# Optimization experiments

Measured on AMD Instinct MI355X. Metric: run time of the kernel, lower is better.

## Reference

```python
import jax, jax.numpy as jnp
import numpy as np

N = 50000
E = 800000
P = 16
H = 128
NUM_LAYERS = 2


def _lin_params(key, fan_in, fan_out):
    k1, k2 = jax.random.split(key)
    bound = 1.0 / np.sqrt(fan_in)
    W = jax.random.uniform(k1, (fan_in, fan_out), jnp.float32, -bound, bound)
    b = jax.random.uniform(k2, (fan_out,), jnp.float32, -bound, bound)
    return W, b


def setup_inputs() -> dict:
    key = jax.random.key(0)
    ks = jax.random.split(key, 16)
    h = jax.random.normal(ks[0], (N, P), jnp.float32)
    x = jax.random.normal(ks[1], (N, 2), jnp.float32)
    edge_index = jax.random.randint(ks[2], (2, E), 0, N, jnp.int32)
    emb_W, emb_b = _lin_params(ks[3], P, H)
    e_W1, e_b1 = _lin_params(ks[4], 2 * H + 1, H)
    e_W2, e_b2 = _lin_params(ks[5], H, H)
    n_W1, n_b1 = _lin_params(ks[6], 2 * H, H)
    n_W2, n_b2 = _lin_params(ks[7], H, H)
    v_W1, v_b1 = _lin_params(ks[8], H, H)
    v_W2, v_b2 = _lin_params(ks[9], H, 2)
    c_W1, c_b1 = _lin_params(ks[10], H, H)
    c_W2, c_b2 = _lin_params(ks[11], H, 1)
    return dict(h=h, x=x, edge_index=edge_index,
                emb_W=emb_W, emb_b=emb_b,
                e_W1=e_W1, e_b1=e_b1, e_W2=e_W2, e_b2=e_b2,
                n_W1=n_W1, n_b1=n_b1, n_W2=n_W2, n_b2=n_b2,
                v_W1=v_W1, v_b1=v_b1, v_W2=v_W2, v_b2=v_b2,
                c_W1=c_W1, c_b1=c_b1, c_W2=c_W2, c_b2=c_b2)


def _mlp(z, W1, b1, W2, b2):
    return jnp.maximum(z @ W1 + b1, 0.0) @ W2 + b2


def reference(h, x, edge_index, emb_W, emb_b,
              e_W1, e_b1, e_W2, e_b2,
              n_W1, n_b1, n_W2, n_b2,
              v_W1, v_b1, v_W2, v_b2,
              c_W1, c_b1, c_W2, c_b2):
    row, col = edge_index[0], edge_index[1]
    n_nodes = h.shape[0]
    # edge count per source node for scatter-mean (0-count nodes stay 0)
    cnt = jax.ops.segment_sum(jnp.ones((row.shape[0],), h.dtype), row,
                              num_segments=n_nodes)
    denom = jnp.maximum(cnt, 1.0)[:, None]

    h = h @ emb_W + emb_b  # [N, H]
    v = None
    for _ in range(NUM_LAYERS):
        rel_pos = x[row] - x[col]                         # [E, 2]
        rel_dist = jnp.sum(rel_pos ** 2, axis=-1, keepdims=True)  # [E, 1]
        rel_theta = jnp.arctan2(rel_pos[:, 1], rel_pos[:, 0])     # [E]
        rel_pos2 = rel_dist * jnp.stack(
            [jnp.cos(2.0 * rel_theta), jnp.sin(2.0 * rel_theta)], axis=1)  # [E, 2]
        edge_feat = jnp.concatenate([h[row], h[col], rel_dist], axis=-1)   # [E, 2H+1]
        m_ij = _mlp(edge_feat, e_W1, e_b1, e_W2, e_b2)    # [E, H] (dropout = eval identity)
        m_i = jax.ops.segment_sum(m_ij, row, num_segments=n_nodes)  # [N, H]
        h = h + _mlp(jnp.concatenate([h, m_i], axis=-1), n_W1, n_b1, n_W2, n_b2)
        v = _mlp(h, v_W1, v_b1, v_W2, v_b2)               # [N, 2]
        coord = _mlp(m_ij, c_W1, c_b1, c_W2, c_b2)        # [E, 1]
        scat = jax.ops.segment_sum(rel_pos2 * coord, row, num_segments=n_nodes)
        v = v + scat / denom                              # scatter-mean
    # F.normalize(p=2, dim=-1, eps=1e-12)
    norm = jnp.linalg.norm(v, axis=-1, keepdims=True)
    v = v / jnp.maximum(norm, 1e-12)
    return h, x, v
```

## Files before the change

### kernel.cpp

```cpp
#include <hip/hip_runtime.h>
#include <hip/hip_fp16.h>

typedef _Float16 f16;
typedef unsigned short u16;
typedef f16 f16x2 __attribute__((ext_vector_type(2)));
typedef f16 f16x8 __attribute__((ext_vector_type(8)));
typedef float f32x4 __attribute__((ext_vector_type(4)));

constexpr int N_NODES = 50000;
constexpr int E_EDGES = 800000;
constexpr int NBINS   = 50176;
constexpr int NBLK    = 196;

constexpr size_t OFF_DEG   = 0;
constexpr size_t OFF_LOCEX = 200704;
constexpr size_t OFF_BSUM  = 401408;
constexpr size_t OFF_BOFF  = 402432;
constexpr size_t OFF_FILL  = 403456;
constexpr size_t OFF_SCAT  = 604160;
constexpr size_t OFF_SROW  = 1004160;
constexpr size_t OFF_SCOL  = 2604160;
constexpr size_t OFF_ZSUM  = 4204160;
constexpr size_t ZSH_BYTES = (size_t)N_NODES * 128 * 2;
constexpr size_t ZS_BYTES  = (size_t)N_NODES * 128 * 4;
constexpr size_t OFF_APRE  = OFF_ZSUM + ZS_BYTES;
constexpr size_t OFF_BPRE  = OFF_APRE + (size_t)N_NODES * 128 * 2;
constexpr size_t OFF_CMB   = OFF_BPRE + (size_t)N_NODES * 128 * 2;
constexpr size_t OFF_WX    = OFF_CMB + 65536;
constexpr size_t OFF_BVEC  = OFF_WX + 65536;
constexpr size_t OFF_BX    = OFF_BVEC + 512;
constexpr size_t OFF_WSWZ  = OFF_BX + 512;

__device__ __forceinline__ void split_f(float x, f16& h, f16& l) {
    h = (f16)x;
    l = (f16)(x - (float)h);
}

__device__ __forceinline__ f32x4 mfma3(f16x8 ah, f16x8 al, f16x8 bh, f16x8 bl, f32x4 acc) {
    acc = __builtin_amdgcn_mfma_f32_16x16x32_f16(ah, bh, acc, 0, 0, 0);
    acc = __builtin_amdgcn_mfma_f32_16x16x32_f16(al, bh, acc, 0, 0, 0);
    acc = __builtin_amdgcn_mfma_f32_16x16x32_f16(ah, bl, acc, 0, 0, 0);
    return acc;
}

__device__ __forceinline__ void pk_atomic_add(f16* addr, float a0, float a1) {
    __half2 hv = __floats2half2_rn(a0, a1);
    unsafeAtomicAdd((__half2*)addr, hv);
}

__global__ __launch_bounds__(256) void compose_kernel(
    const float* __restrict__ eW2, const float* __restrict__ eb2,
    const float* __restrict__ nW1, const float* __restrict__ cW1,
    const float* __restrict__ cb1,
    float* __restrict__ Wcmb, float* __restrict__ Wx,
    float* __restrict__ bvec, float* __restrict__ bx)
{
    const int gid = blockIdx.x * 256 + threadIdx.x;
    if (gid < 16384) {
        const int k = gid >> 7, j = gid & 127;
        float s = 0.f;
        for (int t2 = 0; t2 < 128; ++t2) s += eW2[k * 128 + t2] * nW1[(128 + t2) * 128 + j];
        Wcmb[gid] = s;
    } else if (gid < 32768) {
        const int e = gid - 16384;
        const int k = e >> 7, j = e & 127;
        float s = 0.f;
        for (int t2 = 0; t2 < 128; ++t2) s += eW2[k * 128 + t2] * cW1[t2 * 128 + j];
        Wx[e] = s;
    } else if (gid < 32896) {
        const int j = gid - 32768;
        float s = 0.f;
        for (int k = 0; k < 128; ++k) s += eb2[k] * nW1[(128 + k) * 128 + j];
        bvec[j] = s;
    } else if (gid < 33024) {
        const int j = gid - 32896;
        float s = cb1[j];
        for (int k = 0; k < 128; ++k) s += eb2[k] * cW1[k * 128 + j];
        bx[j] = s;
    }
}

__global__ __launch_bounds__(256) void prep_kernel(
    const float* __restrict__ eW1, const float* __restrict__ nW1,
    const float* __restrict__ nW2, const float* __restrict__ vW1,
    const float* __restrict__ Wcmb, const float* __restrict__ Wx,
    f16* __restrict__ Wpres, f16* __restrict__ nW1cs,
    f16* __restrict__ nW2s, f16* __restrict__ vW1s, f16* __restrict__ Wxs)
{
    const int gid = blockIdx.x * 256 + threadIdx.x;
    int K32, e, which; f16* out;
    if (gid < 32768)       { which = 0; out = Wpres; K32 = 4; e = gid; }
    else if (gid < 65536)  { which = 1; out = nW1cs; K32 = 8; e = gid - 32768; }
    else if (gid < 81920)  { which = 2; out = nW2s;  K32 = 4; e = gid - 65536; }
    else if (gid < 98304)  { which = 3; out = vW1s;  K32 = 4; e = gid - 81920; }
    else                   { which = 4; out = Wxs;   K32 = 4; e = gid - 98304; }
    const int per = 512 * K32;
    const int ct = e / per, rem = e % per;
    const int kk = rem >> 9, lane = (rem >> 3) & 63, j = rem & 7;
    const int col = ct * 16 + (lane & 15);
    const int k = kk * 32 + ((lane >> 4) & 3) * 8 + j;
    float v;
    if (which == 0)      v = (col < 128) ? eW1[k * 128 + col] : eW1[(128 + k) * 128 + (col - 128)];
    else if (which == 1) v = (k < 128) ? nW1[k * 128 + col] : Wcmb[(k - 128) * 128 + col];
    else if (which == 2) v = nW2[k * 128 + col];
    else if (which == 3) v = vW1[k * 128 + col];
    else                 v = Wx[k * 128 + col];
    f16 h, l; split_f(v, h, l);
    const int base = ((ct * K32 + kk) * 2) * 512 + lane * 8 + j;
    out[base] = h;
    out[base + 512] = l;
}

__global__ __launch_bounds__(256) void hist_kernel(const int* __restrict__ eidx,
                                                   int* __restrict__ deg) {
    const int e = blockIdx.x * 256 + threadIdx.x;
    if (e < E_EDGES) atomicAdd(&deg[eidx[e]], 1);
}

__global__ __launch_bounds__(256) void scan1_kernel(const int* __restrict__ deg,
                                                    int* __restrict__ locEx,
                                                    int* __restrict__ blockSum) {
    __shared__ int s[256];
    const int t = threadIdx.x;
    const int gid = blockIdx.x * 256 + t;
    const int v = deg[gid];
    s[t] = v;
    __syncthreads();
    for (int off = 1; off < 256; off <<= 1) {
        const int add = (t >= off) ? s[t - off] : 0;
        __syncthreads();
        s[t] += add;
        __syncthreads();
    }
    locEx[gid] = s[t] - v;
    if (t == 255) blockSum[blockIdx.x] = s[255];
}

__global__ __launch_bounds__(256) void scan2_kernel(const int* __restrict__ blockSum,
                                                    int* __restrict__ blockOff) {
    __shared__ int s[256];
    const int t = threadIdx.x;
    const int v = (t < NBLK) ? blockSum[t] : 0;
    s[t] = v;
    __syncthreads();
    for (int off = 1; off < 256; off <<= 1) {
        const int add = (t >= off) ? s[t - off] : 0;
        __syncthreads();
        s[t] += add;
        __syncthreads();
    }
    if (t < NBLK) blockOff[t] = s[t] - v;
}

__global__ __launch_bounds__(256) void scatter_kernel(const int* __restrict__ eidx,
        const int* __restrict__ locEx, const int* __restrict__ blockOff,
        int* __restrict__ fill, u16* __restrict__ srow, u16* __restrict__ scol) {
    const int e = blockIdx.x * 256 + threadIdx.x;
    if (e >= E_EDGES) return;
    const int r = eidx[e], c = eidx[E_EDGES + e];
    const int pos = blockOff[r >> 8] + locEx[r] + atomicAdd(&fill[r], 1);
    srow[pos] = (u16)r;
    scol[pos] = (u16)c;
}

__global__ __launch_bounds__(256) void embed_kernel(
    const float* __restrict__ h_in, const float* __restrict__ embW,
    const float* __restrict__ embb, float* __restrict__ h)
{
    const int gid = blockIdx.x * 256 + threadIdx.x;
    if (gid >= N_NODES * 128) return;
    const int n = gid >> 7, j = gid & 127;
    float s = embb[j];
#pragma unroll
    for (int p = 0; p < 16; ++p) s += h_in[n * 16 + p] * embW[p * 128 + j];
    h[gid] = s;
}

__device__ __forceinline__ void stage8(const float* src, f16* dst) {
    const float4 f0 = *(const float4*)src;
    const float4 f1 = *(const float4*)(src + 4);
    const float xs[8] = {f0.x, f0.y, f0.z, f0.w, f1.x, f1.y, f1.z, f1.w};
    f16x8 vh, vl;
#pragma unroll
    for (int i = 0; i < 8; ++i) { f16 hh, ll; split_f(xs[i], hh, ll); vh[i] = hh; vl[i] = ll; }
    *(f16x8*)dst = vh;
    *(f16x8*)(dst + 8) = vl;
}

__global__ __launch_bounds__(256, 4) void pre_kernel(
    const float* __restrict__ h, const f16* __restrict__ Wpres,
    const float* __restrict__ eb1,
    f16* __restrict__ Apre, f16* __restrict__ Bpre)
{
    constexpr int S = 264;
    __shared__ f16 smA[64 * S];
    const int t = threadIdx.x;
    const int base = blockIdx.x * 64;
    const int lane = t & 63, w = t >> 6, qq = lane >> 4, nn = lane & 15;

#pragma unroll
    for (int it = 0; it < 4; ++it) {
        const int idx = it * 256 + t;
        const int el = idx >> 4, seg = idx & 15;
        const int node = base + el;
        f16* dst = &smA[el * S + seg * 16];
        if (node < N_NODES) {
            stage8(h + (size_t)node * 128 + seg * 8, dst);
        } else {
            *(f16x8*)dst = (f16x8)(f16)0.f;
            *(f16x8*)(dst + 8) = (f16x8)(f16)0.f;
        }
    }
    __syncthreads();

#pragma unroll
    for (int half = 0; half < 2; ++half) {
        f32x4 acc[4][2] = {};
        for (int kk = 0; kk < 4; ++kk) {
            f16x8 Ah[4], Al[4];
#pragma unroll
            for (int rt = 0; rt < 4; ++rt) {
                const f16* ap = &smA[(rt * 16 + nn) * S + (kk * 4 + qq) * 16];
                Ah[rt] = *(const f16x8*)ap;
                Al[rt] = *(const f16x8*)(ap + 8);
            }
#pragma unroll
            for (int c = 0; c < 2; ++c) {
                const int ct = w * 4 + half * 2 + c;
                const f16* bp = Wpres + (size_t)((ct * 4 + kk) * 2) * 512 + lane * 8;
                const f16x8 Bh = *(const f16x8*)bp;
                const f16x8 Bl = *(const f16x8*)(bp + 512);
#pragma unroll
                for (int rt = 0; rt < 4; ++rt)
                    acc[rt][c] = mfma3(Ah[rt], Al[rt], Bh, Bl, acc[rt][c]);
            }
        }
#pragma unroll
        for (int c = 0; c < 2; ++c) {
            const int col = w * 64 + half * 32 + c * 16 + nn;
#pragma unroll
            for (int rt = 0; rt < 4; ++rt) {
#pragma unroll
                for (int r = 0; r < 4; ++r) {
                    const int el = rt * 16 + qq * 4 + r;
                    const int node = base + el;
                    if (node < N_NODES) {
                        const float v = acc[rt][c][r];
                        if (col < 128) Apre[(size_t)node * 128 + col] = (f16)(v + eb1[col]);
                        else           Bpre[(size_t)node * 128 + (col - 128)] = (f16)v;
                    }
                }
            }
        }
    }
}

__global__ __launch_bounds__(256, 8) void edge_z_kernel(
    const u16* __restrict__ srow, const u16* __restrict__ scol,
    const float* __restrict__ x,
    const f16* __restrict__ Apre, const f16* __restrict__ Bpre,
    const float* __restrict__ wlast,
    f16* __restrict__ zsumh)
{
    constexpr int S2 = 136;
    __shared__ f16 smZ[64 * S2];
    __shared__ int smRow[64], smCol[64];
    __shared__ float smRd[64];
    const int t = threadIdx.x;
    const int base = blockIdx.x * 64;
    if (t < 64) {
        const int e = base + t;
        const int r = (int)srow[e], c = (int)scol[e];
        smRow[t] = r; smCol[t] = c;
        const float dx = x[2 * r] - x[2 * c];
        const float dy = x[2 * r + 1] - x[2 * c + 1];
        smRd[t] = dx * dx + dy * dy;
    }
    __syncthreads();

    const int seg = t & 15;
    const float4 w0 = *(const float4*)(wlast + seg * 8);
    const float4 w1 = *(const float4*)(wlast + seg * 8 + 4);
    const float wl[8] = {w0.x, w0.y, w0.z, w0.w, w1.x, w1.y, w1.z, w1.w};
#pragma unroll
    for (int it = 0; it < 4; ++it) {
        const int el = it * 16 + (t >> 4);
        const int rn = smRow[el], cn = smCol[el];
        const f16x8 av = *(const f16x8*)(Apre + (size_t)rn * 128 + seg * 8);
        const f16x8 bv = *(const f16x8*)(Bpre + (size_t)cn * 128 + seg * 8);
        const float rd = smRd[el];
        f16x8 vz;
#pragma unroll
        for (int i = 0; i < 8; ++i)
            vz[i] = (f16)fmaxf((float)av[i] + (float)bv[i] + rd * wl[i], 0.f);
        *(f16x8*)&smZ[el * S2 + seg * 8] = vz;
    }
    __syncthreads();

    const int p = t & 63, g = t >> 6;
    float a0 = 0.f, a1 = 0.f;
    int prev = smRow[g * 16];
#pragma unroll
    for (int e = g * 16; e < g * 16 + 16; ++e) {
        const int rw = smRow[e];
        if (rw != prev) {
            pk_atomic_add(&zsumh[(size_t)prev * 128 + 2 * p], a0, a1);
            a0 = a1 = 0.f; prev = rw;
        }
        const f16x2 v = *(const f16x2*)&smZ[e * S2 + 2 * p];
        a0 += (float)v[0]; a1 += (float)v[1];
    }
    pk_atomic_add(&zsumh[(size_t)prev * 128 + 2 * p], a0, a1);
}

__global__ __launch_bounds__(256, 8) void edge_coord_kernel(
    const u16* __restrict__ srow, const u16* __restrict__ scol,
    const float* __restrict__ x,
    const f16* __restrict__ Apre, const f16* __restrict__ Bpre,
    const float* __restrict__ wlast,
    const f16* __restrict__ Wxs, const float* __restrict__ bx,
    const float* __restrict__ cW2, const float* __restrict__ cb2,
    f16* __restrict__ zsumh, float* __restrict__ scat)
{
    constexpr int S2 = 136;
    __shared__ f16 smZ[64 * S2];
    __shared__ int smRow[64], smCol[64];
    __shared__ float smRd[64], smP2x[64], smP2y[64];
    __shared__ float smPart[4][64];

    const int t = threadIdx.x;
    const int base = blockIdx.x * 64;
    const int lane = t & 63, w = t >> 6, qq = lane >> 4, nn = lane & 15;

    if (t < 64) {
        const int e = base + t;
        const int r = (int)srow[e], c = (int)scol[e];
        smRow[t] = r; smCol[t] = c;
        const float dx = x[2 * r] - x[2 * c];
        const float dy = x[2 * r + 1] - x[2 * c + 1];
        smRd[t] = dx * dx + dy * dy;
        smP2x[t] = dx * dx - dy * dy;
        smP2y[t] = 2.0f * dx * dy;
    }
    __syncthreads();

    {
        const int seg = t & 15;
        const float4 w0 = *(const float4*)(wlast + seg * 8);
        const float4 w1 = *(const float4*)(wlast + seg * 8 + 4);
        const float wl[8] = {w0.x, w0.y, w0.z, w0.w, w1.x, w1.y, w1.z, w1.w};
#pragma unroll
        for (int it = 0; it < 4; ++it) {
            const int el = it * 16 + (t >> 4);
            const int rn = smRow[el], cn = smCol[el];
            const f16x8 av = *(const f16x8*)(Apre + (size_t)rn * 128 + seg * 8);
            const f16x8 bv = *(const f16x8*)(Bpre + (size_t)cn * 128 + seg * 8);
            const float rd = smRd[el];
            f16x8 vz;
#pragma unroll
            for (int i = 0; i < 8; ++i)
                vz[i] = (f16)fmaxf((float)av[i] + (float)bv[i] + rd * wl[i], 0.f);
            *(f16x8*)&smZ[el * S2 + seg * 8] = vz;
        }
    }
    __syncthreads();

    {
        const int p = t & 63, g = t >> 6;
        float a0 = 0.f, a1 = 0.f;
        int prev = smRow[g * 16];
#pragma unroll
        for (int e = g * 16; e < g * 16 + 16; ++e) {
            const int rw = smRow[e];
            if (rw != prev) {
                pk_atomic_add(&zsumh[(size_t)prev * 128 + 2 * p], a0, a1);
                a0 = a1 = 0.f; prev = rw;
            }
            const f16x2 v = *(const f16x2*)&smZ[e * S2 + 2 * p];
            a0 += (float)v[0]; a1 += (float)v[1];
        }
        pk_atomic_add(&zsumh[(size_t)prev * 128 + 2 * p], a0, a1);
    }

    f32x4 acc3[4][2] = {};
    for (int kk = 0; kk < 4; ++kk) {
        f16x8 A[4];
#pragma unroll
        for (int rt = 0; rt < 4; ++rt)
            A[rt] = *(const f16x8*)&smZ[(rt * 16 + nn) * S2 + (kk * 4 + qq) * 8];
#pragma unroll
        for (int c = 0; c < 2; ++c) {
            const int ct = w * 2 + c;
            const f16x8 Bh = *(const f16x8*)(Wxs + (size_t)((ct * 4 + kk) * 2) * 512 + lane * 8);
#pragma unroll
            for (int rt = 0; rt < 4; ++rt)
                acc3[rt][c] = __builtin_amdgcn_mfma_f32_16x16x32_f16(A[rt], Bh, acc3[rt][c], 0, 0, 0);
        }
    }
    float p3[4][4];
#pragma unroll
    for (int rt = 0; rt < 4; ++rt)
#pragma unroll
        for (int r = 0; r < 4; ++r) p3[rt][r] = 0.f;
#pragma unroll
    for (int c = 0; c < 2; ++c) {
        const int col = w * 32 + c * 16 + nn;
        const float c1 = bx[col];
        const float w2 = cW2[col];
#pragma unroll
        for (int rt = 0; rt < 4; ++rt)
#pragma unroll
            for (int r = 0; r < 4; ++r)
                p3[rt][r] += fmaxf(acc3[rt][c][r] + c1, 0.f) * w2;
    }
#pragma unroll
    for (int off = 1; off < 16; off <<= 1)
#pragma unroll
        for (int rt = 0; rt < 4; ++rt)
#pragma unroll
            for (int r = 0; r < 4; ++r) p3[rt][r] += __shfl_xor(p3[rt][r], off);
    if (nn == 0) {
#pragma unroll
        for (int rt = 0; rt < 4; ++rt)
#pragma unroll
            for (int r = 0; r < 4; ++r)
                smPart[w][rt * 16 + qq * 4 + r] = p3[rt][r];
    }
    __syncthreads();
    if (t < 64) {
        const float co = smPart[0][t] + smPart[1][t] + smPart[2][t] + smPart[3][t] + cb2[0];
        const int rw = smRow[t];
        atomicAdd(&scat[2 * rw],     smP2x[t] * co);
        atomicAdd(&scat[2 * rw + 1], smP2y[t] * co);
    }
}

__device__ __forceinline__ void node_core(
    float* __restrict__ h, f16* __restrict__ zsumh,
    const int* __restrict__ deg,
    const f16* __restrict__ nW1cs, const float* __restrict__ nb1,
    const float* __restrict__ bvec,
    const f16* __restrict__ nW2s, const float* __restrict__ nb2,
    f16* smA, float* smDeg, int t, int base)
{
    constexpr int S = 264;
    const int lane = t & 63, w = t >> 6, qq = lane >> 4, nn = lane & 15;

    if (t < 64) smDeg[t] = (float)deg[base + t];

    f32x4 acc1[4][2] = {};
    for (int chunk = 0; chunk < 2; ++chunk) {
        if (chunk) __syncthreads();
#pragma unroll
        for (int it = 0; it < 4; ++it) {
            const int idx = it * 256 + t;
            const int el = idx >> 4, seg = idx & 15;
            const int node = base + el;
            f16* dst = &smA[el * S + seg * 16];
            if (node < N_NODES) {
                if (chunk == 0) {
                    stage8(h + (size_t)node * 128 + seg * 8, dst);
                } else {
                    f16* src = zsumh + (size_t)node * 128 + seg * 8;
                    const f16x8 v = *(const f16x8*)src;
                    *(f16x8*)dst = v;
                    *(f16x8*)(dst + 8) = (f16x8)(f16)0.f;
                    *(f16x8*)src = (f16x8)(f16)0.f;
                }
            } else {
                *(f16x8*)dst = (f16x8)(f16)0.f;
                *(f16x8*)(dst + 8) = (f16x8)(f16)0.f;
            }
        }
        __syncthreads();
        for (int kk = 0; kk < 4; ++kk) {
            f16x8 Ah[4], Al[4];
#pragma unroll
            for (int rt = 0; rt < 4; ++rt) {
                const f16* ap = &smA[(rt * 16 + nn) * S + (kk * 4 + qq) * 16];
                Ah[rt] = *(const f16x8*)ap;
                Al[rt] = *(const f16x8*)(ap + 8);
            }
            const int kkg = chunk * 4 + kk;
#pragma unroll
            for (int c = 0; c < 2; ++c) {
                const int ct = w * 2 + c;
                const f16* bp = nW1cs + (size_t)((ct * 8 + kkg) * 2) * 512 + lane * 8;
                const f16x8 Bh = *(const f16x8*)bp;
                const f16x8 Bl = *(const f16x8*)(bp + 512);
#pragma unroll
                for (int rt = 0; rt < 4; ++rt)
                    acc1[rt][c] = mfma3(Ah[rt], Al[rt], Bh, Bl, acc1[rt][c]);
            }
        }
    }
    __syncthreads();
#pragma unroll
    for (int c = 0; c < 2; ++c) {
        const int col = w * 32 + c * 16 + nn;
        const float b1 = nb1[col];
        const float bv = bvec[col];
#pragma unroll
        for (int rt = 0; rt < 4; ++rt) {
#pragma unroll
            for (int r = 0; r < 4; ++r) {
                const int el = rt * 16 + qq * 4 + r;
                const float z = fmaxf(acc1[rt][c][r] + b1 + smDeg[el] * bv, 0.f);
                f16 zh, zl; split_f(z, zh, zl);
                f16* zp = &smA[el * S + (col >> 3) * 16 + (col & 7)];
                zp[0] = zh; zp[8] = zl;
            }
        }
    }
    __syncthreads();

    f32x4 acc2[4][2] = {};
    for (int kk = 0; kk < 4; ++kk) {
        f16x8 Ah[4], Al[4];
#pragma unroll
        for (int rt = 0; rt < 4; ++rt) {
            const f16* ap = &smA[(rt * 16 + nn) * S + (kk * 4 + qq) * 16];
            Ah[rt] = *(const f16x8*)ap;
            Al[rt] = *(const f16x8*)(ap + 8);
        }
#pragma unroll
        for (int c = 0; c < 2; ++c) {
            const int ct = w * 2 + c;
            const f16* bp = nW2s + (size_t)((ct * 4 + kk) * 2) * 512 + lane * 8;
            const f16x8 Bh = *(const f16x8*)bp;
            const f16x8 Bl = *(const f16x8*)(bp + 512);
#pragma unroll
            for (int rt = 0; rt < 4; ++rt)
                acc2[rt][c] = mfma3(Ah[rt], Al[rt], Bh, Bl, acc2[rt][c]);
        }
    }
    __syncthreads();
#pragma unroll
    for (int c = 0; c < 2; ++c) {
        const int col = w * 32 + c * 16 + nn;
        const float b2 = nb2[col];
#pragma unroll
        for (int rt = 0; rt < 4; ++rt) {
#pragma unroll
            for (int r = 0; r < 4; ++r) {
                const int el = rt * 16 + qq * 4 + r;
                const int node = base + el;
                if (node < N_NODES) {
                    const size_t ix = (size_t)node * 128 + col;
                    const float hn = h[ix] + acc2[rt][c][r] + b2;
                    h[ix] = hn;
                    f16 hh, hl; split_f(hn, hh, hl);
                    f16* hp = &smA[el * S + (col >> 3) * 16 + (col & 7)];
                    hp[0] = hh; hp[8] = hl;
                }
            }
        }
    }
    __syncthreads();
}

__global__ __launch_bounds__(256, 4) void node_pre_kernel(
    float* __restrict__ h, f16* __restrict__ zsumh,
    const int* __restrict__ deg,
    const f16* __restrict__ nW1cs, const float* __restrict__ nb1,
    const float* __restrict__ bvec,
    const f16* __restrict__ nW2s, const float* __restrict__ nb2,
    const f16* __restrict__ Wpres, const float* __restrict__ eb1,
    f16* __restrict__ Apre, f16* __restrict__ Bpre)
{
    constexpr int S = 264;
    __shared__ f16 smA[64 * S];
    __shared__ float smDeg[64];
    const int t = threadIdx.x;
    const int base = blockIdx.x * 64;
    const int lane = t & 63, w = t >> 6, qq = lane >> 4, nn = lane & 15;

    node_core(h, zsumh, deg, nW1cs, nb1, bvec, nW2s, nb2, smA, smDeg, t, base);

#pragma unroll
    for (int half = 0; half < 2; ++half) {
        f32x4 acc[4][2] = {};
        for (int kk = 0; kk < 4; ++kk) {
            f16x8 Ah[4], Al[4];
#pragma unroll
            for (int rt = 0; rt < 4; ++rt) {
                const f16* ap = &smA[(rt * 16 + nn) * S + (kk * 4 + qq) * 16];
                Ah[rt] = *(const f16x8*)ap;
                Al[rt] = *(const f16x8*)(ap + 8);
            }
#pragma unroll
            for (int c = 0; c < 2; ++c) {
                const int ct = w * 4 + half * 2 + c;
                const f16* bp = Wpres + (size_t)((ct * 4 + kk) * 2) * 512 + lane * 8;
                const f16x8 Bh = *(const f16x8*)bp;
                const f16x8 Bl = *(const f16x8*)(bp + 512);
#pragma unroll
                for (int rt = 0; rt < 4; ++rt)
                    acc[rt][c] = mfma3(Ah[rt], Al[rt], Bh, Bl, acc[rt][c]);
            }
        }
#pragma unroll
        for (int c = 0; c < 2; ++c) {
            const int col = w * 64 + half * 32 + c * 16 + nn;
#pragma unroll
            for (int rt = 0; rt < 4; ++rt) {
#pragma unroll
                for (int r = 0; r < 4; ++r) {
                    const int el = rt * 16 + qq * 4 + r;
                    const int node = base + el;
                    if (node < N_NODES) {
                        const float v = acc[rt][c][r];
                        if (col < 128) Apre[(size_t)node * 128 + col] = (f16)(v + eb1[col]);
                        else           Bpre[(size_t)node * 128 + (col - 128)] = (f16)v;
                    }
                }
            }
        }
    }
}

__global__ __launch_bounds__(256, 4) void node_final_kernel(
    float* __restrict__ h, f16* __restrict__ zsumh,
    const int* __restrict__ deg,
    const f16* __restrict__ nW1cs, const float* __restrict__ nb1,
    const float* __restrict__ bvec,
    const f16* __restrict__ nW2s, const float* __restrict__ nb2,
    const f16* __restrict__ vW1s, const float* __restrict__ vb1,
    const float* __restrict__ vW2, const float* __restrict__ vb2,
    const float* __restrict__ scat, const float* __restrict__ x,
    float* __restrict__ out)
{
    constexpr int S = 264;
    __shared__ f16 smA[64 * S];
    __shared__ float smDeg[64];
    const int t = threadIdx.x;
    const int base = blockIdx.x * 64;
    const int lane = t & 63, w = t >> 6, qq = lane >> 4, nn = lane & 15;

    node_core(h, zsumh, deg, nW1cs, nb1, bvec, nW2s, nb2, smA, smDeg, t, base);

    f32x4 acc1[4][2] = {};
    for (int kk = 0; kk < 4; ++kk) {
        f16x8 Ah[4], Al[4];
#pragma unroll
        for (int rt = 0; rt < 4; ++rt) {
            const f16* ap = &smA[(rt * 16 + nn) * S + (kk * 4 + qq) * 16];
            Ah[rt] = *(const f16x8*)ap;
            Al[rt] = *(const f16x8*)(ap + 8);
        }
#pragma unroll
        for (int c = 0; c < 2; ++c) {
            const int ct = w * 2 + c;
            const f16* bp = vW1s + (size_t)((ct * 4 + kk) * 2) * 512 + lane * 8;
            const f16x8 Bh = *(const f16x8*)bp;
            const f16x8 Bl = *(const f16x8*)(bp + 512);
#pragma unroll
            for (int rt = 0; rt < 4; ++rt)
                acc1[rt][c] = mfma3(Ah[rt], Al[rt], Bh, Bl, acc1[rt][c]);
        }
    }
    __syncthreads();
#pragma unroll
    for (int c = 0; c < 2; ++c) {
        const int col = w * 32 + c * 16 + nn;
        const float b1 = vb1[col];
#pragma unroll
        for (int rt = 0; rt < 4; ++rt) {
#pragma unroll
            for (int r = 0; r < 4; ++r) {
                const int el = rt * 16 + qq * 4 + r;
                const float z = fmaxf(acc1[rt][c][r] + b1, 0.f);
                f16 zh, zl; split_f(z, zh, zl);
                f16* zp = &smA[el * S + (col >> 3) * 16 + (col & 7)];
                zp[0] = zh; zp[8] = zl;
            }
        }
    }
    __syncthreads();

    float* out_x = out + (size_t)N_NODES * 128;
    float* out_v = out_x + (size_t)N_NODES * 2;
    if (t < 128) {
        const int node = base + (t >> 1);
        if (node < N_NODES) out_x[node * 2 + (t & 1)] = x[node * 2 + (t & 1)];
    }
    if (t < 128) {
        const int rl = t >> 1, comp = t & 1;
        const int node = base + rl;
        float s = 0.f;
        if (node < N_NODES) {
            s = vb2[comp];
            for (int k = 0; k < 128; ++k) {
                const f16* zp = &smA[rl * S + (k >> 3) * 16 + (k & 7)];
                const float z = (float)zp[0] + (float)zp[8];
                s += z * vW2[k * 2 + comp];
            }
            const float dn = fmaxf((float)smDeg[rl], 1.0f);
            s += scat[node * 2 + comp] / dn;
        }
        const float other = __shfl_xor(s, 1);
        if (node < N_NODES) {
            const float nrm = sqrtf(s * s + other * other);
            out_v[node * 2 + comp] = s / fmaxf(nrm, 1e-12f);
        }
    }
}

extern "C" void kernel_launch(void* const* d_in, const int* in_sizes, int n_in,
                              void* d_out, int out_size, void* d_ws, size_t ws_size,
                              hipStream_t stream) {
    const float* h_in = (const float*)d_in[0];
    const float* x    = (const float*)d_in[1];
    const int*   eidx = (const int*)d_in[2];
    const float* embW = (const float*)d_in[3];
    const float* embb = (const float*)d_in[4];
    const float* eW1  = (const float*)d_in[5];
    const float* eb1  = (const float*)d_in[6];
    const float* eW2  = (const float*)d_in[7];
    const float* eb2  = (const float*)d_in[8];
    const float* nW1  = (const float*)d_in[9];
    const float* nb1  = (const float*)d_in[10];
    const float* nW2  = (const float*)d_in[11];
    const float* nb2  = (const float*)d_in[12];
    const float* vW1  = (const float*)d_in[13];
    const float* vb1  = (const float*)d_in[14];
    const float* vW2  = (const float*)d_in[15];
    const float* vb2  = (const float*)d_in[16];
    const float* cW1  = (const float*)d_in[17];
    const float* cb1  = (const float*)d_in[18];
    const float* cW2  = (const float*)d_in[19];
    const float* cb2  = (const float*)d_in[20];

    char* ws = (char*)d_ws;
    int* deg    = (int*)(ws + OFF_DEG);
    int* locEx  = (int*)(ws + OFF_LOCEX);
    int* bsum   = (int*)(ws + OFF_BSUM);
    int* boff   = (int*)(ws + OFF_BOFF);
    int* fill   = (int*)(ws + OFF_FILL);
    float* scat = (float*)(ws + OFF_SCAT);
    u16* srow   = (u16*)(ws + OFF_SROW);
    u16* scol   = (u16*)(ws + OFF_SCOL);
    f16* zsumh  = (f16*)(ws + OFF_ZSUM);
    f16* Apre   = (f16*)(ws + OFF_APRE);
    f16* Bpre   = (f16*)(ws + OFF_BPRE);
    float* Wcmb = (float*)(ws + OFF_CMB);
    float* Wx   = (float*)(ws + OFF_WX);
    float* bvec = (float*)(ws + OFF_BVEC);
    float* bx   = (float*)(ws + OFF_BX);
    f16* Wpres  = (f16*)(ws + OFF_WSWZ);
    f16* nW1cs  = Wpres + 65536;
    f16* nW2s   = nW1cs + 65536;
    f16* vW1s   = nW2s + 32768;
    f16* Wxs    = vW1s + 32768;

    float* hcur = (float*)d_out;

    hipMemsetAsync(ws, 0, OFF_SROW, stream);
    hipMemsetAsync(zsumh, 0, ZSH_BYTES, stream);

    compose_kernel<<<129, 256, 0, stream>>>(eW2, eb2, nW1, cW1, cb1, Wcmb, Wx, bvec, bx);
    prep_kernel<<<448, 256, 0, stream>>>(eW1, nW1, nW2, vW1, Wcmb, Wx,
                                         Wpres, nW1cs, nW2s, vW1s, Wxs);
    hist_kernel<<<(E_EDGES + 255) / 256, 256, 0, stream>>>(eidx, deg);
    scan1_kernel<<<NBLK, 256, 0, stream>>>(deg, locEx, bsum);
    scan2_kernel<<<1, 256, 0, stream>>>(bsum, boff);
    scatter_kernel<<<(E_EDGES + 255) / 256, 256, 0, stream>>>(eidx, locEx, boff,
                                                              fill, srow, scol);
    embed_kernel<<<(N_NODES * 128 + 255) / 256, 256, 0, stream>>>(h_in, embW, embb, hcur);

    const float* wlast = eW1 + 256 * 128;

    pre_kernel<<<(N_NODES + 63) / 64, 256, 0, stream>>>(hcur, Wpres, eb1, Apre, Bpre);
    edge_z_kernel<<<E_EDGES / 64, 256, 0, stream>>>(srow, scol, x, Apre, Bpre, wlast, zsumh);
    node_pre_kernel<<<(N_NODES + 63) / 64, 256, 0, stream>>>(hcur, zsumh, deg,
        nW1cs, nb1, bvec, nW2s, nb2, Wpres, eb1, Apre, Bpre);

    edge_coord_kernel<<<E_EDGES / 64, 256, 0, stream>>>(srow, scol, x, Apre, Bpre, wlast,
        Wxs, bx, cW2, cb2, zsumh, scat);
    node_final_kernel<<<(N_NODES + 63) / 64, 256, 0, stream>>>(hcur, zsumh, deg,
        nW1cs, nb1, bvec, nW2s, nb2, vW1s, vb1, vW2, vb2, scat, x, (float*)d_out);
}
```

Before: 583.9 us.

## Replace edge-parallel atomic z-sum with node-parallel CSR gather

The first-layer edge aggregation now assigns 16 threads to each source node and walks that node's CSR edge range, which it locates from the exclusive scan and block offsets. Sums are kept in fp32 registers and written once, with no packed fp16 atomics and no shared-memory staging. The sorted srow array is no longer needed in this kernel, and the loads of the row's Apre slice and x coordinates are hoisted out of the edge loop. The trade-off is load imbalance from varying node degrees and a serial per-node loop with limited parallelism per thread group.

```diff
diff --git a/kernel.cpp b/kernel.cpp
--- a/kernel.cpp
+++ b/kernel.cpp
@@ -255,62 +255,61 @@
     }
 }
 
-__global__ __launch_bounds__(256, 8) void edge_z_kernel(
-    const u16* __restrict__ srow, const u16* __restrict__ scol,
+__global__ __launch_bounds__(256, 8) void edge_z_nc_kernel(
+    const u16* __restrict__ scol,
+    const int* __restrict__ locEx, const int* __restrict__ boff,
+    const int* __restrict__ deg,
     const float* __restrict__ x,
     const f16* __restrict__ Apre, const f16* __restrict__ Bpre,
     const float* __restrict__ wlast,
     f16* __restrict__ zsumh)
 {
-    constexpr int S2 = 136;
-    __shared__ f16 smZ[64 * S2];
-    __shared__ int smRow[64], smCol[64];
-    __shared__ float smRd[64];
     const int t = threadIdx.x;
-    const int base = blockIdx.x * 64;
-    if (t < 64) {
-        const int e = base + t;
-        const int r = (int)srow[e], c = (int)scol[e];
-        smRow[t] = r; smCol[t] = c;
-        const float dx = x[2 * r] - x[2 * c];
-        const float dy = x[2 * r + 1] - x[2 * c + 1];
-        smRd[t] = dx * dx + dy * dy;
-    }
-    __syncthreads();
-
-    const int seg = t & 15;
+    const int seg = t & 15, g = t >> 4;
+    const int r = blockIdx.x * 16 + g;
+    if (r >= N_NODES) return;
+    const int rs  = boff[r >> 8] + locEx[r];
+    const int cnt = deg[r];
+    const float xr0 = x[2 * r], xr1 = x[2 * r + 1];
+    const f16x8 av = *(const f16x8*)(Apre + (size_t)r * 128 + seg * 8);
     const float4 w0 = *(const float4*)(wlast + seg * 8);
     const float4 w1 = *(const float4*)(wlast + seg * 8 + 4);
     const float wl[8] = {w0.x, w0.y, w0.z, w0.w, w1.x, w1.y, w1.z, w1.w};
-#pragma unroll
-    for (int it = 0; it < 4; ++it) {
-        const int el = it * 16 + (t >> 4);
-        const int rn = smRow[el], cn = smCol[el];
-        const f16x8 av = *(const f16x8*)(Apre + (size_t)rn * 128 + seg * 8);
-        const f16x8 bv = *(const f16x8*)(Bpre + (size_t)cn * 128 + seg * 8);
-        const float rd = smRd[el];
-        f16x8 vz;
-#pragma unroll
-        for (int i = 0; i < 8; ++i)
-            vz[i] = (f16)fmaxf((float)av[i] + (float)bv[i] + rd * wl[i], 0.f);
-        *(f16x8*)&smZ[el * S2 + seg * 8] = vz;
-    }
-    __syncthreads();
-
-    const int p = t & 63, g = t >> 6;
-    float a0 = 0.f, a1 = 0.f;
-    int prev = smRow[g * 16];
-#pragma unroll
-    for (int e = g * 16; e < g * 16 + 16; ++e) {
-        const int rw = smRow[e];
-        if (rw != prev) {
-            pk_atomic_add(&zsumh[(size_t)prev * 128 + 2 * p], a0, a1);
-            a0 = a1 = 0.f; prev = rw;
-        }
-        const f16x2 v = *(const f16x2*)&smZ[e * S2 + 2 * p];
-        a0 += (float)v[0]; a1 += (float)v[1];
-    }
-    pk_atomic_add(&zsumh[(size_t)prev * 128 + 2 * p], a0, a1);
+
+    float acc[8] = {0.f, 0.f, 0.f, 0.f, 0.f, 0.f, 0.f, 0.f};
+    int i = 0;
+    for (; i + 4 <= cnt; i += 4) {
+        int c4[4];
+#pragma unroll
+        for (int j = 0; j < 4; ++j) c4[j] = (int)scol[rs + i + j];
+        f16x8 bv4[4]; float rd4[4];
+#pragma unroll
+        for (int j = 0; j < 4; ++j) {
+            bv4[j] = *(const f16x8*)(Bpre + (size_t)c4[j] * 128 + seg * 8);
+            const float dx = xr0 - x[2 * c4[j]];
+            const float dy = xr1 - x[2 * c4[j] + 1];
+            rd4[j] = dx * dx + dy * dy;
+        }
+#pragma unroll
+        for (int j = 0; j < 4; ++j)
+#pragma unroll
+            for (int k = 0; k < 8; ++k)
+                acc[k] += fmaxf((float)av[k] + (float)bv4[j][k] + rd4[j] * wl[k], 0.f);
+    }
+    for (; i < cnt; ++i) {
+        const int c = (int)scol[rs + i];
+        const f16x8 bv = *(const f16x8*)(Bpre + (size_t)c * 128 + seg * 8);
+        const float dx = xr0 - x[2 * c];
+        const float dy = xr1 - x[2 * c + 1];
+        const float rd = dx * dx + dy * dy;
+#pragma unroll
+        for (int k = 0; k < 8; ++k)
+            acc[k] += fmaxf((float)av[k] + (float)bv[k] + rd * wl[k], 0.f);
+    }
+    f16x8 outz;
+#pragma unroll
+    for (int k = 0; k < 8; ++k) outz[k] = (f16)acc[k];
+    *(f16x8*)(zsumh + (size_t)r * 128 + seg * 8) = outz;
 }
 
 __global__ __launch_bounds__(256, 8) void edge_coord_kernel(
@@ -771,7 +770,8 @@
     const float* wlast = eW1 + 256 * 128;
 
     pre_kernel<<<(N_NODES + 63) / 64, 256, 0, stream>>>(hcur, Wpres, eb1, Apre, Bpre);
-    edge_z_kernel<<<E_EDGES / 64, 256, 0, stream>>>(srow, scol, x, Apre, Bpre, wlast, zsumh);
+    edge_z_nc_kernel<<<(N_NODES + 15) / 16, 256, 0, stream>>>(scol, locEx, boff, deg,
+        x, Apre, Bpre, wlast, zsumh);
     node_pre_kernel<<<(N_NODES + 63) / 64, 256, 0, stream>>>(hcur, zsumh, deg,
         nW1cs, nb1, bvec, nW2s, nb2, Wpres, eb1, Apre, Bpre);
 
```

Result: no change. 590.3 us (+1.1%).
